# Kernel optimization log

Hardware: AMD Instinct MI355X
Metric: run time of the kernel (lower is better)

## Reference

```python
import jax, jax.numpy as jnp
import numpy as np
import math

B = 256        # batch of series
V = 1024       # vocabulary size (Vocabulary not given; modeled as V random words)
SIZE = 1024    # self.size
CELL = 8       # self.cell_size == word length
SEQ = SIZE // CELL   # 128 segments
DMODEL = 768
NHAAR = 8      # int(log2(128)) + 1
THRESH = 0.95


def _pos_emb():
    position = np.arange(SEQ, dtype=np.float32)[:, None]
    div = np.exp(np.arange(0, DMODEL, 2, dtype=np.float32) * (-math.log(10000.0) / DMODEL))
    pe = np.zeros((SEQ, DMODEL), np.float32)
    pe[:, 0::2] = np.sin(position * div)
    pe[:, 1::2] = np.cos(position * div)
    return jnp.asarray(pe)


def setup_inputs() -> dict:
    key = jax.random.key(0)
    k1, k2, k3, k4 = jax.random.split(key, 4)
    return {
        "X": jax.random.normal(k1, (B, SIZE), jnp.float32),
        "vocab": jax.random.normal(k2, (V, CELL), jnp.float32),
        "word_emb": jax.random.normal(k3, (V, DMODEL), jnp.float32),
        "haar_emb": jax.random.normal(k4, (NHAAR, DMODEL), jnp.float32),
        "pos_emb": _pos_emb(),
    }


def _select(corr):
    """Replicates get_sequence's sequential update over vocabulary order.
    Stored best is the SIGNED correlation c (faithful to the original code),
    compared against |c_new|; accept when |c_new| > threshold and best < |c_new|.
    corr: [B, V, S] -> idx [B, S] (int32, -1 = no word selected)."""
    cs = jnp.transpose(corr, (1, 0, 2))  # [V, B, S]

    def step(carry, xs):
        best, idx = carry
        c, i = xs
        a = jnp.abs(c)
        take = (a > THRESH) & (best < a)
        return (jnp.where(take, c, best), jnp.where(take, i, idx)), None

    init = (jnp.full((corr.shape[0], corr.shape[2]), -jnp.inf, corr.dtype),
            jnp.full((corr.shape[0], corr.shape[2]), -1, jnp.int32))
    (_, idx), _ = jax.lax.scan(step, init, (cs, jnp.arange(V, dtype=jnp.int32)))
    return idx


def _haar_details(x):
    """pywt 'haar' detail coeffs: ds[k] = cD_{k+1}, cD = (x_even - x_odd)/sqrt(2)."""
    inv = jnp.float32(1.0 / math.sqrt(2.0))
    a = x
    ds = []
    for _ in range(10):  # log2(1024) levels
        ds.append((a[:, ::2] - a[:, 1::2]) * inv)
        a = (a[:, ::2] + a[:, 1::2]) * inv
    return ds


def reference(X, vocab, word_emb, haar_emb, pos_emb):
    # --- per-segment cross-correlation against every vocabulary word ---
    seg = X.reshape(B, SEQ, CELL)
    seg_c = seg - seg.mean(-1, keepdims=True)
    seg_std = jnp.sqrt((seg_c * seg_c).mean(-1))          # population std, [B,S]
    w_c = vocab - vocab.mean(-1, keepdims=True)
    w_std = jnp.sqrt((w_c * w_c).mean(-1))                # [V]
    cov = jnp.einsum('bsc,vc->bvs', seg_c, w_c) / CELL    # [B,V,S]
    denom = w_std[None, :, None] * seg_std[:, None, :]
    corr = jnp.where(denom == 0, 0.0, cov / jnp.where(denom == 0, 1.0, denom))

    idx = _select(corr)                                   # [B,S]
    mask = (idx >= 0)

    # --- word embedding lookup (zeros where no word passed threshold) ---
    we = word_emb[jnp.clip(idx, 0, V - 1)] * mask[..., None].astype(word_emb.dtype)

    # --- Haar wavelet coefficients, levels cD_10 .. cD_3 (lengths 1..128) ---
    ds = _haar_details(X)
    pos = jnp.arange(SEQ)
    cols = []
    for l in range(NHAAR):                                # haar_coeffs[l] = cD_{10-l}
        gi = (pos * (2 ** l)) // SEQ                      # i // (SEQ / 2**l)
        cols.append(ds[9 - l][:, gi])                     # [B,S]
    hc = jnp.stack(cols, axis=-1) * mask[..., None].astype(X.dtype)  # [B,S,8]
    haar = jnp.einsum('bsh,hd->bsd', hc, haar_emb)        # [B,S,768]

    return we + pos_emb[None] + haar                      # [B,128,768]
```

## Files before the change

kernel.cpp:

```cpp
#include <hip/hip_runtime.h>
#include <math.h>

#define THRESH_ 0.95f

typedef float nfloat4 __attribute__((ext_vector_type(4)));
typedef __attribute__((ext_vector_type(8))) short short8v;
typedef __attribute__((ext_vector_type(16))) float f32x16;

__device__ __forceinline__ unsigned short f2bf_rne(float x) {
    unsigned u = __float_as_uint(x);
    u += 0x7fffu + ((u >> 16) & 1u);
    return (unsigned short)(u >> 16);
}

__global__ __launch_bounds__(1024) void k12_fused(const float* __restrict__ X,
                                                  const float* __restrict__ vocab,
                                                  const float* __restrict__ word_emb,
                                                  const float* __restrict__ haar_emb,
                                                  const float* __restrict__ pos_emb,
                                                  float* __restrict__ out) {
    __shared__ float4  wcl4[2048];
    __shared__ short8v wcb_lds[1024];
    __shared__ float   wsl[1024];
    __shared__ float   xrow[1024];
    __shared__ float   segf[1024];
    __shared__ short8v segb[128];
    __shared__ float   sstd_l[128];
    __shared__ float   thr_l[128];
    __shared__ float   stb[512];
    __shared__ int     sti[512];
    __shared__ float   stm[512];
    __shared__ float   tree[254];
    __shared__ float   hc_lds[1024];
    __shared__ int     idx_lds[128];

    int t = threadIdx.x;
    int b = blockIdx.x;

    xrow[t] = X[b * 1024 + t];
    {
        const float4* v4 = (const float4*)vocab + t * 2;
        float4 a = v4[0], bb = v4[1];
        float w[8] = {a.x, a.y, a.z, a.w, bb.x, bb.y, bb.z, bb.w};
        float s = 0.f;
#pragma unroll
        for (int c = 0; c < 8; c++) s += w[c];
        float mean = s * 0.125f;
        float ss = 0.f;
        float wcv[8];
#pragma unroll
        for (int c = 0; c < 8; c++) { wcv[c] = w[c] - mean; ss += wcv[c] * wcv[c]; }
        float sd = sqrtf(ss * 0.125f);
        float4 o0 = {wcv[0], wcv[1], wcv[2], wcv[3]};
        float4 o1 = {wcv[4], wcv[5], wcv[6], wcv[7]};
        wcl4[t * 2] = o0;
        wcl4[t * 2 + 1] = o1;
        wsl[t] = sd;
        union { uint4 q; unsigned short u[8]; } pk;
#pragma unroll
        for (int c = 0; c < 8; c++) pk.u[c] = f2bf_rne(wcv[c]);
        ((uint4*)wcb_lds)[t] = pk.q;
    }
    if (t < 512) { stb[t] = -INFINITY; sti[t] = -1; stm[t] = 0.f; }
    __syncthreads();

    if (t < 128) {
        float seg[8];
#pragma unroll
        for (int c = 0; c < 8; c++) seg[c] = xrow[t * 8 + c];
        float sum = 0.f;
#pragma unroll
        for (int c = 0; c < 8; c++) sum += seg[c];
        float mean = sum * 0.125f;
        float segc[8];
        float ss = 0.f;
#pragma unroll
        for (int c = 0; c < 8; c++) { segc[c] = seg[c] - mean; ss += segc[c] * segc[c]; }
        float sstd = sqrtf(ss * 0.125f);
        union { short8v v; unsigned short u[8]; } pk;
#pragma unroll
        for (int c = 0; c < 8; c++) { segf[t * 8 + c] = segc[c]; pk.u[c] = f2bf_rne(segc[c]); }
        segb[t] = pk.v;
        sstd_l[t] = sstd;
        thr_l[t] = 7.52f * sstd;
        tree[t] = sum;
    }
    __syncthreads();

    int w = t >> 6, lane = t & 63;
    {
        int sb = w & 3;
        int g = w >> 2;
        int half = lane >> 5;

        short8v af = {0, 0, 0, 0, 0, 0, 0, 0};
        if (lane < 32) af = segb[sb * 32 + lane];

        float thr_r[16];
#pragma unroll
        for (int i = 0; i < 16; i++) {
            int row = (i & 3) + 8 * (i >> 2) + 4 * half;
            thr_r[i] = thr_l[sb * 32 + row];
        }

        const double MID = 0x1.E66667p-1;
        for (int j = 0; j < 8; j++) {
            int wb = g * 8 + j;
            short8v bf = {0, 0, 0, 0, 0, 0, 0, 0};
            if (lane < 32) bf = wcb_lds[wb * 32 + lane];
            float wsd_c = wsl[wb * 32 + (lane & 31)];

            f32x16 accz = {0.f, 0.f, 0.f, 0.f, 0.f, 0.f, 0.f, 0.f,
                           0.f, 0.f, 0.f, 0.f, 0.f, 0.f, 0.f, 0.f};
            f32x16 acc = __builtin_amdgcn_mfma_f32_32x32x16_bf16(af, bf, accz, 0, 0, 0);

            bool anyp = false;
#pragma unroll
            for (int i = 0; i < 16; i++) anyp |= (fabsf(acc[i]) > thr_r[i] * wsd_c);

            if (__builtin_expect(anyp, 0)) {
#pragma unroll
                for (int i = 0; i < 16; i++) {
                    unsigned long long mi = __ballot(fabsf(acc[i]) > thr_r[i] * wsd_c);
                    while (mi) {
                        int src = __builtin_ctzll(mi);
                        mi &= mi - 1;
                        if (lane == src) {
                            int col = src & 31;
                            int seg_r = sb * 32 + (i & 3) + 8 * (i >> 2) + 4 * (src >> 5);
                            int v = wb * 32 + col;
                            float sst = sstd_l[seg_r];
                            float wsd = wsl[v];
                            const float* sc = &segf[seg_r * 8];
                            float4 wa = wcl4[v * 2];
                            float4 wbv = wcl4[v * 2 + 1];
                            float dot = sc[0] * wa.x + sc[1] * wa.y + sc[2] * wa.z + sc[3] * wa.w
                                      + sc[4] * wbv.x + sc[5] * wbv.y + sc[6] * wbv.z + sc[7] * wbv.w;
                            float cov = dot * 0.125f;
                            float denom = wsd * sst;
                            if ((double)fabsf(cov) >= MID * (double)denom) {
                                float c = (denom == 0.f) ? 0.f : cov / denom;
                                float a = fabsf(c);
                                int sidx = g * 128 + seg_r;
                                stm[sidx] = fmaxf(stm[sidx], a);
                                if (a > THRESH_ && stb[sidx] < a) { stb[sidx] = c; sti[sidx] = v; }
                            }
                        }
                    }
                }
            }
        }
    }
    __syncthreads();

    if (t < 64) tree[128 + t] = tree[2 * t] + tree[2 * t + 1];
    __syncthreads();
    if (t < 32) tree[192 + t] = tree[128 + 2 * t] + tree[128 + 2 * t + 1];
    __syncthreads();
    if (t < 16) tree[224 + t] = tree[192 + 2 * t] + tree[192 + 2 * t + 1];
    __syncthreads();
    if (t < 8) tree[240 + t] = tree[224 + 2 * t] + tree[224 + 2 * t + 1];
    __syncthreads();
    if (t < 4) tree[248 + t] = tree[240 + 2 * t] + tree[240 + 2 * t + 1];
    __syncthreads();
    if (t < 2) tree[252 + t] = tree[248 + 2 * t] + tree[248 + 2 * t + 1];
    __syncthreads();

    if (t < 128) {
        float Bb = stb[t];
        int I = sti[t];
#pragma unroll
        for (int p = 1; p < 4; p++) {
            float yb = stb[p * 128 + t];
            int yi = sti[p * 128 + t];
            float ym = stm[p * 128 + t];
            bool take = (yi != -1) && (!(Bb > THRESH_) || (ym > Bb));
            if (take) { Bb = yb; I = yi; }
        }
        float mask = (I >= 0) ? 1.f : 0.f;

        const int base[7] = {252, 248, 240, 224, 192, 128, 0};
        const float scl[7] = {0.03125f, 0.04419417382415922f, 0.0625f,
                              0.08838834764831843f, 0.125f,
                              0.17677669529663687f, 0.25f};
        float hcv[8];
#pragma unroll
        for (int l = 0; l < 7; l++) {
            int j = (t << l) >> 7;
            hcv[l] = scl[l] * (tree[base[l] + 2 * j] - tree[base[l] + 2 * j + 1]);
        }
        float s4a = xrow[t * 8 + 0] + xrow[t * 8 + 1] + xrow[t * 8 + 2] + xrow[t * 8 + 3];
        float s4b = xrow[t * 8 + 4] + xrow[t * 8 + 5] + xrow[t * 8 + 6] + xrow[t * 8 + 7];
        hcv[7] = 0.3535533905932738f * (s4a - s4b);

#pragma unroll
        for (int l = 0; l < 8; l++) hc_lds[t * 8 + l] = hcv[l] * mask;
        idx_lds[t] = I;
    }
    __syncthreads();

    if (w < 12) {
        int third = w % 3;
        int grp = w / 3;
        int c = third * 64 + lane;

        float4 he[8];
        const float4* hg = (const float4*)haar_emb;
#pragma unroll
        for (int l = 0; l < 8; l++) he[l] = hg[l * 192 + c];

        const float4* pos4 = (const float4*)pos_emb;
        const float4* we4 = (const float4*)word_emb;
        float4* out4 = (float4*)out + (size_t)b * 128 * 192;

        for (int k = 0; k < 32; k += 2) {
            int row0 = grp * 32 + k;
            int row1 = row0 + 1;
            int iv0 = idx_lds[row0];
            int iv1 = idx_lds[row1];
            int ivc0 = iv0 < 0 ? 0 : iv0;
            int ivc1 = iv1 < 0 ? 0 : iv1;
            float msk0 = iv0 < 0 ? 0.f : 1.f;
            float msk1 = iv1 < 0 ? 0.f : 1.f;
            float4 p0 = pos4[row0 * 192 + c];
            float4 w0 = we4[(size_t)ivc0 * 192 + c];
            float4 h0a = *(const float4*)&hc_lds[row0 * 8];
            float4 h0b = *(const float4*)&hc_lds[row0 * 8 + 4];
            float4 p1 = pos4[row1 * 192 + c];
            float4 w1 = we4[(size_t)ivc1 * 192 + c];
            float4 h1a = *(const float4*)&hc_lds[row1 * 8];
            float4 h1b = *(const float4*)&hc_lds[row1 * 8 + 4];

            float4 acc0;
            acc0.x = fmaf(w0.x, msk0, p0.x);
            acc0.y = fmaf(w0.y, msk0, p0.y);
            acc0.z = fmaf(w0.z, msk0, p0.z);
            acc0.w = fmaf(w0.w, msk0, p0.w);
            float h0[8] = {h0a.x, h0a.y, h0a.z, h0a.w, h0b.x, h0b.y, h0b.z, h0b.w};
#pragma unroll
            for (int l = 0; l < 8; l++) {
                acc0.x += h0[l] * he[l].x;
                acc0.y += h0[l] * he[l].y;
                acc0.z += h0[l] * he[l].z;
                acc0.w += h0[l] * he[l].w;
            }
            {
                nfloat4 nv = {acc0.x, acc0.y, acc0.z, acc0.w};
                __builtin_nontemporal_store(nv, (nfloat4*)&out4[row0 * 192 + c]);
            }

            float4 acc1;
            acc1.x = fmaf(w1.x, msk1, p1.x);
            acc1.y = fmaf(w1.y, msk1, p1.y);
            acc1.z = fmaf(w1.z, msk1, p1.z);
            acc1.w = fmaf(w1.w, msk1, p1.w);
            float h1[8] = {h1a.x, h1a.y, h1a.z, h1a.w, h1b.x, h1b.y, h1b.z, h1b.w};
#pragma unroll
            for (int l = 0; l < 8; l++) {
                acc1.x += h1[l] * he[l].x;
                acc1.y += h1[l] * he[l].y;
                acc1.z += h1[l] * he[l].z;
                acc1.w += h1[l] * he[l].w;
            }
            {
                nfloat4 nv = {acc1.x, acc1.y, acc1.z, acc1.w};
                __builtin_nontemporal_store(nv, (nfloat4*)&out4[row1 * 192 + c]);
            }
        }
    }
}

extern "C" void kernel_launch(void* const* d_in, const int* in_sizes, int n_in,
                              void* d_out, int out_size, void* d_ws, size_t ws_size,
                              hipStream_t stream) {
    const float* X        = (const float*)d_in[0];
    const float* vocab    = (const float*)d_in[1];
    const float* word_emb = (const float*)d_in[2];
    const float* haar_emb = (const float*)d_in[3];
    const float* pos_emb  = (const float*)d_in[4];
    float* out = (float*)d_out;

    hipLaunchKernelGGL(k12_fused, dim3(256), dim3(1024), 0, stream,
                       X, vocab, word_emb, haar_emb, pos_emb, out);
}
```

Before: 35.65 us.

## Split each batch row across two blocks by segment halves

```diff
diff --git a/kernel.cpp b/kernel.cpp
--- a/kernel.cpp
+++ b/kernel.cpp
@@ -13,29 +13,31 @@
     return (unsigned short)(u >> 16);
 }
 
-__global__ __launch_bounds__(1024) void k12_fused(const float* __restrict__ X,
-                                                  const float* __restrict__ vocab,
-                                                  const float* __restrict__ word_emb,
-                                                  const float* __restrict__ haar_emb,
-                                                  const float* __restrict__ pos_emb,
-                                                  float* __restrict__ out) {
+__global__ __launch_bounds__(1024, 8) void k12_fused(const float* __restrict__ X,
+                                                     const float* __restrict__ vocab,
+                                                     const float* __restrict__ word_emb,
+                                                     const float* __restrict__ haar_emb,
+                                                     const float* __restrict__ pos_emb,
+                                                     float* __restrict__ out) {
     __shared__ float4  wcl4[2048];
     __shared__ short8v wcb_lds[1024];
     __shared__ float   wsl[1024];
     __shared__ float   xrow[1024];
-    __shared__ float   segf[1024];
-    __shared__ short8v segb[128];
-    __shared__ float   sstd_l[128];
-    __shared__ float   thr_l[128];
+    __shared__ float   segf[512];
+    __shared__ short8v segb[64];
+    __shared__ float   sstd_l[64];
+    __shared__ float   thr_l[64];
     __shared__ float   stb[512];
     __shared__ int     sti[512];
     __shared__ float   stm[512];
     __shared__ float   tree[254];
-    __shared__ float   hc_lds[1024];
-    __shared__ int     idx_lds[128];
+    __shared__ float   hc_lds[512];
+    __shared__ int     idx_lds[64];
 
     int t = threadIdx.x;
-    int b = blockIdx.x;
+    int bid = blockIdx.x;
+    int b = bid >> 1;
+    int h = bid & 1;
 
     xrow[t] = X[b * 1024 + t];
     {
@@ -71,26 +73,29 @@
         float sum = 0.f;
 #pragma unroll
         for (int c = 0; c < 8; c++) sum += seg[c];
-        float mean = sum * 0.125f;
-        float segc[8];
-        float ss = 0.f;
-#pragma unroll
-        for (int c = 0; c < 8; c++) { segc[c] = seg[c] - mean; ss += segc[c] * segc[c]; }
-        float sstd = sqrtf(ss * 0.125f);
-        union { short8v v; unsigned short u[8]; } pk;
-#pragma unroll
-        for (int c = 0; c < 8; c++) { segf[t * 8 + c] = segc[c]; pk.u[c] = f2bf_rne(segc[c]); }
-        segb[t] = pk.v;
-        sstd_l[t] = sstd;
-        thr_l[t] = 7.52f * sstd;
         tree[t] = sum;
+        int local = t - h * 64;
+        if (local >= 0 && local < 64) {
+            float mean = sum * 0.125f;
+            float segc[8];
+            float ss = 0.f;
+#pragma unroll
+            for (int c = 0; c < 8; c++) { segc[c] = seg[c] - mean; ss += segc[c] * segc[c]; }
+            float sstd = sqrtf(ss * 0.125f);
+            union { short8v v; unsigned short u[8]; } pk;
+#pragma unroll
+            for (int c = 0; c < 8; c++) { segf[local * 8 + c] = segc[c]; pk.u[c] = f2bf_rne(segc[c]); }
+            segb[local] = pk.v;
+            sstd_l[local] = sstd;
+            thr_l[local] = 7.52f * sstd;
+        }
     }
     __syncthreads();
 
     int w = t >> 6, lane = t & 63;
     {
-        int sb = w & 3;
-        int g = w >> 2;
+        int sb = w & 1;
+        int g = w >> 1;
         int half = lane >> 5;
 
         short8v af = {0, 0, 0, 0, 0, 0, 0, 0};
@@ -104,8 +109,8 @@
         }
 
         const double MID = 0x1.E66667p-1;
-        for (int j = 0; j < 8; j++) {
-            int wb = g * 8 + j;
+        for (int j = 0; j < 4; j++) {
+            int wb = g * 4 + j;
             short8v bf = {0, 0, 0, 0, 0, 0, 0, 0};
             if (lane < 32) bf = wcb_lds[wb * 32 + lane];
             float wsd_c = wsl[wb * 32 + (lane & 31)];
@@ -141,7 +146,7 @@
                             if ((double)fabsf(cov) >= MID * (double)denom) {
                                 float c = (denom == 0.f) ? 0.f : cov / denom;
                                 float a = fabsf(c);
-                                int sidx = g * 128 + seg_r;
+                                int sidx = g * 64 + seg_r;
                                 stm[sidx] = fmaxf(stm[sidx], a);
                                 if (a > THRESH_ && stb[sidx] < a) { stb[sidx] = c; sti[sidx] = v; }
                             }
@@ -166,19 +171,20 @@
     if (t < 2) tree[252 + t] = tree[248 + 2 * t] + tree[248 + 2 * t + 1];
     __syncthreads();
 
-    if (t < 128) {
+    if (t < 64) {
         float Bb = stb[t];
         int I = sti[t];
 #pragma unroll
-        for (int p = 1; p < 4; p++) {
-            float yb = stb[p * 128 + t];
-            int yi = sti[p * 128 + t];
-            float ym = stm[p * 128 + t];
+        for (int p = 1; p < 8; p++) {
+            float yb = stb[p * 64 + t];
+            int yi = sti[p * 64 + t];
+            float ym = stm[p * 64 + t];
             bool take = (yi != -1) && (!(Bb > THRESH_) || (ym > Bb));
             if (take) { Bb = yb; I = yi; }
         }
         float mask = (I >= 0) ? 1.f : 0.f;
 
+        int sg = h * 64 + t;
         const int base[7] = {252, 248, 240, 224, 192, 128, 0};
         const float scl[7] = {0.03125f, 0.04419417382415922f, 0.0625f,
                               0.08838834764831843f, 0.125f,
@@ -186,11 +192,11 @@
         float hcv[8];
 #pragma unroll
         for (int l = 0; l < 7; l++) {
-            int j = (t << l) >> 7;
+            int j = (sg << l) >> 7;
             hcv[l] = scl[l] * (tree[base[l] + 2 * j] - tree[base[l] + 2 * j + 1]);
         }
-        float s4a = xrow[t * 8 + 0] + xrow[t * 8 + 1] + xrow[t * 8 + 2] + xrow[t * 8 + 3];
-        float s4b = xrow[t * 8 + 4] + xrow[t * 8 + 5] + xrow[t * 8 + 6] + xrow[t * 8 + 7];
+        float s4a = xrow[sg * 8 + 0] + xrow[sg * 8 + 1] + xrow[sg * 8 + 2] + xrow[sg * 8 + 3];
+        float s4b = xrow[sg * 8 + 4] + xrow[sg * 8 + 5] + xrow[sg * 8 + 6] + xrow[sg * 8 + 7];
         hcv[7] = 0.3535533905932738f * (s4a - s4b);
 
 #pragma unroll
@@ -211,10 +217,10 @@
 
         const float4* pos4 = (const float4*)pos_emb;
         const float4* we4 = (const float4*)word_emb;
-        float4* out4 = (float4*)out + (size_t)b * 128 * 192;
-
-        for (int k = 0; k < 32; k += 2) {
-            int row0 = grp * 32 + k;
+        float4* out4 = (float4*)out + ((size_t)b * 128 + h * 64) * 192;
+
+        for (int k = 0; k < 16; k += 2) {
+            int row0 = grp * 16 + k;
             int row1 = row0 + 1;
             int iv0 = idx_lds[row0];
             int iv1 = idx_lds[row1];
@@ -222,11 +228,12 @@
             int ivc1 = iv1 < 0 ? 0 : iv1;
             float msk0 = iv0 < 0 ? 0.f : 1.f;
             float msk1 = iv1 < 0 ? 0.f : 1.f;
-            float4 p0 = pos4[row0 * 192 + c];
+            int sg0 = h * 64 + row0, sg1 = h * 64 + row1;
+            float4 p0 = pos4[sg0 * 192 + c];
             float4 w0 = we4[(size_t)ivc0 * 192 + c];
             float4 h0a = *(const float4*)&hc_lds[row0 * 8];
             float4 h0b = *(const float4*)&hc_lds[row0 * 8 + 4];
-            float4 p1 = pos4[row1 * 192 + c];
+            float4 p1 = pos4[sg1 * 192 + c];
             float4 w1 = we4[(size_t)ivc1 * 192 + c];
             float4 h1a = *(const float4*)&hc_lds[row1 * 8];
             float4 h1b = *(const float4*)&hc_lds[row1 * 8 + 4];
@@ -280,6 +287,6 @@
     const float* pos_emb  = (const float*)d_in[4];
     float* out = (float*)d_out;
 
-    hipLaunchKernelGGL(k12_fused, dim3(256), dim3(1024), 0, stream,
+    hipLaunchKernelGGL(k12_fused, dim3(512), dim3(1024), 0, stream,
                        X, vocab, word_emb, haar_emb, pos_emb, out);
 }
```

Result: slower. 75.30 us (+111.2%).
